# Performance work log

Measured on AMD Instinct MI355X. Metric: run time of the kernel, lower is better.

Reference implementation:

```python
import jax, jax.numpy as jnp
import numpy as np

GAMMA = 1.0
ALPHA = 0.5
EMBED_DIM = 256
N = 8192
M = 8192


def setup_inputs() -> dict:
    key = jax.random.key(0)
    k1, k2, k3, k4 = jax.random.split(key, 4)
    a = jax.random.normal(k1, (N, EMBED_DIM), dtype=jnp.float32)
    b = jax.random.normal(k2, (M, EMBED_DIM), dtype=jnp.float32)
    # torch.nn.Linear default init: U(-1/sqrt(fan_in), 1/sqrt(fan_in))
    lim = 1.0 / np.sqrt(EMBED_DIM)
    Wq = jax.random.uniform(k3, (EMBED_DIM, EMBED_DIM), jnp.float32, -lim, lim)
    Wk = jax.random.uniform(k4, (EMBED_DIM, EMBED_DIM), jnp.float32, -lim, lim)
    return {"a": a, "b": b, "Wq": Wq, "Wk": Wk}


def reference(a, b, Wq, Wk):
    # Vectorized Gram matrix of HybridKernelMethod.forward over all (a_i, b_j) pairs.
    inv_sqrt_d = np.float32(1.0 / np.sqrt(EMBED_DIM))
    ab = a @ b.T                                           # [N, M] cross dot products
    # RBF part: ||a_i - b_j||^2 = ||a_i||^2 + ||b_j||^2 - 2 a_i.b_j
    sq = (jnp.sum(a * a, axis=-1)[:, None]
          + jnp.sum(b * b, axis=-1)[None, :] - 2.0 * ab)
    rbf_sim = jnp.exp(-GAMMA * sq)                         # [N, M]
    # Attention part: per pair, q k^T is a 1x1 matrix, so softmax == 1 exactly.
    q = a @ Wq.T                                           # [N, D]
    k = b @ Wk.T                                           # [M, D]
    s = (q @ k.T) * inv_sqrt_d                             # [N, M] scores
    scores = jax.nn.softmax(s[..., None], axis=-1)[..., 0]  # all-ones, faithful to 1x1 softmax
    attn_sim = scores * ab                                 # sum((scores @ v) * x) == scores * (a.b)
    return (1.0 - ALPHA) * rbf_sim + ALPHA * attn_sim      # [N, M] Gram matrix
```

## Files before the change

kernel.cpp:

```cpp
#include <hip/hip_runtime.h>
#include <stdint.h>

#define DIM 256
#define NR 8192
#define BM 128
#define BN 128
#define BK 64
#define TPB 8
#define GRID 512

typedef __bf16 bf16x8 __attribute__((ext_vector_type(8)));
typedef float  f32x16 __attribute__((ext_vector_type(16)));
typedef float  f32x4  __attribute__((ext_vector_type(4)));

#define MEMFENCE asm volatile("" ::: "memory")
#define WAITV(N) asm volatile("s_waitcnt vmcnt(" #N ")" ::: "memory")

__device__ __forceinline__ unsigned short f2bf_rne(float f) {
    unsigned int u = __float_as_uint(f);
    u += 0x7FFFu + ((u >> 16) & 1u);
    return (unsigned short)(u >> 16);
}

__global__ void prep_kernel(const float* __restrict__ a,
                            const float* __restrict__ b,
                            unsigned short* __restrict__ aB,
                            unsigned short* __restrict__ bB,
                            float* __restrict__ na,
                            float* __restrict__ nb) {
    const int w = threadIdx.x >> 6;
    const int l = threadIdx.x & 63;
    const int blk = blockIdx.x;
    const float* src; unsigned short* dst; float* nrm; int row;
    if (blk < 2048) { src = a; dst = aB; nrm = na; row = blk * 4 + w; }
    else            { src = b; dst = bB; nrm = nb; row = (blk - 2048) * 4 + w; }
    const float4 v = reinterpret_cast<const float4*>(src + (size_t)row * DIM)[l];
    float ss = v.x * v.x + v.y * v.y + v.z * v.z + v.w * v.w;
#pragma unroll
    for (int off = 32; off > 0; off >>= 1) ss += __shfl_down(ss, off);
    if (l == 0) nrm[row] = ss;
    ushort4 o = make_ushort4(f2bf_rne(v.x), f2bf_rne(v.y), f2bf_rne(v.z), f2bf_rne(v.w));
    reinterpret_cast<ushort4*>(dst + (size_t)row * DIM)[l] = o;
}

#define STAGE(row0_, kt_, buf_)                                                   \
    do {                                                                          \
        _Pragma("unroll")                                                         \
        for (int it_ = 0; it_ < 4; ++it_) {                                       \
            __builtin_amdgcn_global_load_lds(                                     \
                (const __attribute__((address_space(1))) void*)(aB +              \
                    (size_t)((row0_) + rowIt[it_]) * DIM + (kt_) * BK + colIt[it_]), \
                (__attribute__((address_space(3))) void*)&sA[buf_][(w * 4 + it_) * 512], \
                16, 0, 0);                                                        \
        }                                                                         \
        _Pragma("unroll")                                                         \
        for (int it_ = 0; it_ < 4; ++it_) {                                       \
            __builtin_amdgcn_global_load_lds(                                     \
                (const __attribute__((address_space(1))) void*)(bB +              \
                    (size_t)(col0 + rowIt[it_]) * DIM + (kt_) * BK + colIt[it_]), \
                (__attribute__((address_space(3))) void*)&sB[buf_][(w * 4 + it_) * 512], \
                16, 0, 0);                                                        \
        }                                                                         \
    } while (0)

#define COMPUTE(buf_)                                                             \
    do {                                                                          \
        _Pragma("unroll")                                                         \
        for (int ks_ = 0; ks_ < 4; ++ks_) {                                       \
            bf16x8 af[2], bfv[2];                                                 \
            _Pragma("unroll")                                                     \
            for (int mi_ = 0; mi_ < 2; ++mi_)                                     \
                af[mi_] = *(const bf16x8*)((const char*)&sA[buf_][0] +            \
                    baseA[mi_] + ((XA[mi_] ^ (ks_ << 1)) << 4));                  \
            _Pragma("unroll")                                                     \
            for (int ni_ = 0; ni_ < 2; ++ni_)                                     \
                bfv[ni_] = *(const bf16x8*)((const char*)&sB[buf_][0] +           \
                    baseB[ni_] + ((XB[ni_] ^ (ks_ << 1)) << 4));                  \
            _Pragma("unroll")                                                     \
            for (int mi_ = 0; mi_ < 2; ++mi_)                                     \
                _Pragma("unroll")                                                 \
                for (int ni_ = 0; ni_ < 2; ++ni_)                                 \
                    acc[mi_][ni_] = __builtin_amdgcn_mfma_f32_32x32x16_bf16(      \
                        af[mi_], bfv[ni_], acc[mi_][ni_], 0, 0, 0);               \
        }                                                                         \
    } while (0)

__global__ __launch_bounds__(256, 2) void gemm_kernel(
        const unsigned short* __restrict__ aB,
        const unsigned short* __restrict__ bB,
        const float* __restrict__ na,
        const float* __restrict__ nb,
        float* __restrict__ out) {
    __shared__ unsigned short sA[2][8192];
    __shared__ unsigned short sB[2][8192];

    const int t = threadIdx.x;
    const int w = t >> 6, l = t & 63;
    const int wr = w >> 1, wc = w & 1;
    const int hi = l >> 5, lr = l & 31;

    const int bx = (int)blockIdx.x & 63;
    const int bb = (int)blockIdx.x >> 6;
    const int col0 = bx * BN;

    int rowIt[4], colIt[4];
#pragma unroll
    for (int it = 0; it < 4; ++it) {
        int G = (w * 4 + it) * 64 + l;
        int rp = G >> 4, pos = G & 15;
        int c2 = pos ^ (rp & 15);
        rowIt[it] = 2 * rp + (c2 >> 3);
        colIt[it] = (c2 & 7) * 8;
    }
    int baseA[2], XA[2], baseB[2], XB[2];
#pragma unroll
    for (int mi = 0; mi < 2; ++mi) {
        int r = wr * 64 + mi * 32 + lr;
        baseA[mi] = (r >> 1) * 256;
        XA[mi] = (((r & 1) * 8) | hi) ^ ((r >> 1) & 15);
        int rb = wc * 64 + mi * 32 + lr;
        baseB[mi] = (rb >> 1) * 256;
        XB[mi] = (((rb & 1) * 8) | hi) ^ ((rb >> 1) & 15);
    }

    float nbv[2];
#pragma unroll
    for (int ni = 0; ni < 2; ++ni) nbv[ni] = nb[col0 + wc * 64 + ni * 32 + lr];

    float outB[2][16];
    f32x4 nav[2][4];

    {
        const int r0 = bb * BM;
        STAGE(r0, 0, 0);
        STAGE(r0, 1, 1);
    }
    MEMFENCE;

    for (int ti = 0; ti < TPB; ++ti) {
        const int row0 = (bb + ti * 8) * BM;
        f32x16 acc[2][2];
#pragma unroll
        for (int mi = 0; mi < 2; ++mi)
#pragma unroll
            for (int ni = 0; ni < 2; ++ni) acc[mi][ni] = (f32x16)0.0f;

        if (ti == 0) { WAITV(0); } else { WAITV(32); }
        __builtin_amdgcn_s_barrier(); MEMFENCE;
        COMPUTE(0);
        MEMFENCE; __builtin_amdgcn_s_barrier(); MEMFENCE;
        STAGE(row0, 2, 0);
        MEMFENCE;
        if (ti > 0) {
            const int prow = row0 - 1024 + wr * 64 + 32 + 4 * hi;
            const int pcol = col0 + wc * 64 + lr;
#pragma unroll
            for (int ni = 0; ni < 2; ++ni)
#pragma unroll
                for (int tt = 0; tt < 16; ++tt) {
                    int q = tt & 3, p = tt >> 2;
                    __builtin_nontemporal_store(outB[ni][tt],
                        &out[(size_t)(prow + 8 * p + q) * 8192 + pcol + ni * 32]);
                }
        }
        MEMFENCE;

        __builtin_amdgcn_s_barrier(); MEMFENCE;
        COMPUTE(1);
        MEMFENCE; __builtin_amdgcn_s_barrier(); MEMFENCE;
        STAGE(row0, 3, 1);
        MEMFENCE;

        if (ti == 0) { WAITV(8); } else { WAITV(40); }
        __builtin_amdgcn_s_barrier(); MEMFENCE;
        COMPUTE(0);
        MEMFENCE; __builtin_amdgcn_s_barrier(); MEMFENCE;
#pragma unroll
        for (int mi = 0; mi < 2; ++mi)
#pragma unroll
            for (int p = 0; p < 4; ++p)
                nav[mi][p] = *(const f32x4*)&na[row0 + wr * 64 + mi * 32 + 8 * p + 4 * hi];
        MEMFENCE;
        if (ti < TPB - 1) STAGE(row0 + 1024, 0, 0);
        MEMFENCE;

        if (ti == TPB - 1) { WAITV(8); } else { WAITV(16); }
        __builtin_amdgcn_s_barrier(); MEMFENCE;
        COMPUTE(1);
        MEMFENCE; __builtin_amdgcn_s_barrier(); MEMFENCE;
        if (ti < TPB - 1) STAGE(row0 + 1024, 1, 1);
        MEMFENCE;

#pragma unroll
        for (int mi = 0; mi < 2; ++mi)
#pragma unroll
            for (int ni = 0; ni < 2; ++ni)
#pragma unroll
                for (int tt = 0; tt < 16; ++tt) {
                    int q = tt & 3, p = tt >> 2;
                    int row = row0 + wr * 64 + mi * 32 + 8 * p + 4 * hi + q;
                    int col = col0 + wc * 64 + ni * 32 + lr;
                    float dot = acc[mi][ni][tt];
                    float sq = nav[mi][p][q] + nbv[ni] - 2.0f * dot;
                    float v = 0.5f * __expf(-sq) + 0.5f * dot;
                    if (mi == 0)
                        __builtin_nontemporal_store(v, &out[(size_t)row * 8192 + col]);
                    else
                        outB[ni][tt] = v;
                }
        MEMFENCE;
    }

    {
        const int prow = (bb + 56) * BM + wr * 64 + 32 + 4 * hi;
        const int pcol = col0 + wc * 64 + lr;
#pragma unroll
        for (int ni = 0; ni < 2; ++ni)
#pragma unroll
            for (int tt = 0; tt < 16; ++tt) {
                int q = tt & 3, p = tt >> 2;
                __builtin_nontemporal_store(outB[ni][tt],
                    &out[(size_t)(prow + 8 * p + q) * 8192 + pcol + ni * 32]);
            }
    }
}

__global__ void naive_kernel(const float* __restrict__ a,
                             const float* __restrict__ b,
                             float* __restrict__ out) {
    const size_t idx = (size_t)blockIdx.x * 256 + threadIdx.x;
    const int i = (int)(idx >> 13);
    const int j = (int)(idx & 8191);
    float dot = 0.f, naa = 0.f, nbb = 0.f;
    for (int k = 0; k < DIM; ++k) {
        const float x = a[(size_t)i * DIM + k];
        const float y = b[(size_t)j * DIM + k];
        dot += x * y; naa += x * x; nbb += y * y;
    }
    const float sq = naa + nbb - 2.0f * dot;
    out[idx] = 0.5f * __expf(-sq) + 0.5f * dot;
}

extern "C" void kernel_launch(void* const* d_in, const int* in_sizes, int n_in,
                              void* d_out, int out_size, void* d_ws, size_t ws_size,
                              hipStream_t stream) {
    const float* a = (const float*)d_in[0];
    const float* b = (const float*)d_in[1];
    float* out = (float*)d_out;

    const size_t bf_bytes = (size_t)NR * DIM * sizeof(unsigned short);
    const size_t nrm_bytes = (size_t)NR * sizeof(float);
    const size_t need = 2 * bf_bytes + 2 * nrm_bytes;

    if (ws_size >= need) {
        unsigned short* aBf = (unsigned short*)d_ws;
        unsigned short* bBf = (unsigned short*)((char*)d_ws + bf_bytes);
        float* na = (float*)((char*)d_ws + 2 * bf_bytes);
        float* nb = (float*)((char*)d_ws + 2 * bf_bytes + nrm_bytes);

        prep_kernel<<<4096, 256, 0, stream>>>(a, b, aBf, bBf, na, nb);
        gemm_kernel<<<GRID, 256, 0, stream>>>(aBf, bBf, na, nb, out);
    } else {
        naive_kernel<<<((size_t)NR * NR) / 256, 256, 0, stream>>>(a, b, out);
    }
}
```

Measured before the change: 77.17 us.

## Defer all output stores into next tile's K-steps and preload row norms to LDS

All four output sub-tiles are now buffered in registers and written out in chunks interleaved after each of the next tile's four compute phases, instead of storing half immediately. Row norms for all tiles of a block are loaded once into LDS at kernel start, replacing per-tile global loads. MFMA sections are wrapped in s_setprio to favour compute waves. The aim is to spread the large output write traffic evenly across the MFMA work. In exchange, register pressure rises (64 buffered floats) and the vmcnt wait counts are retuned by hand, which risks waiting on the wrong loads if miscounted.

```diff
diff --git a/kernel.cpp b/kernel.cpp
--- a/kernel.cpp
+++ b/kernel.cpp
@@ -15,6 +15,7 @@
 
 #define MEMFENCE asm volatile("" ::: "memory")
 #define WAITV(N) asm volatile("s_waitcnt vmcnt(" #N ")" ::: "memory")
+#define BAR __builtin_amdgcn_s_barrier()
 
 __device__ __forceinline__ unsigned short f2bf_rne(float f) {
     unsigned int u = __float_as_uint(f);
@@ -65,6 +66,7 @@
 
 #define COMPUTE(buf_)                                                             \
     do {                                                                          \
+        __builtin_amdgcn_s_setprio(1);                                            \
         _Pragma("unroll")                                                         \
         for (int ks_ = 0; ks_ < 4; ++ks_) {                                       \
             bf16x8 af[2], bfv[2];                                                 \
@@ -83,6 +85,20 @@
                     acc[mi_][ni_] = __builtin_amdgcn_mfma_f32_32x32x16_bf16(      \
                         af[mi_], bfv[ni_], acc[mi_][ni_], 0, 0, 0);               \
         }                                                                         \
+        __builtin_amdgcn_s_setprio(0);                                            \
+    } while (0)
+
+#define STORE_CHUNK(c_, base_)                                                    \
+    do {                                                                          \
+        const int mi_ = (c_) >> 1, ni_ = (c_) & 1;                                \
+        const int prow_ = (base_) + wr * 64 + mi_ * 32 + 4 * hi;                  \
+        const int pcol_ = col0 + wc * 64 + ni_ * 32 + lr;                         \
+        _Pragma("unroll")                                                         \
+        for (int tt_ = 0; tt_ < 16; ++tt_) {                                      \
+            const int q_ = tt_ & 3, p_ = tt_ >> 2;                                \
+            __builtin_nontemporal_store(outB[c_][tt_],                            \
+                &out[(size_t)(prow_ + 8 * p_ + q_) * 8192 + pcol_]);              \
+        }                                                                         \
     } while (0)
 
 __global__ __launch_bounds__(256, 2) void gemm_kernel(
@@ -93,6 +109,7 @@
         float* __restrict__ out) {
     __shared__ unsigned short sA[2][8192];
     __shared__ unsigned short sB[2][8192];
+    __shared__ float sNA[1024];
 
     const int t = threadIdx.x;
     const int w = t >> 6, l = t & 63;
@@ -127,14 +144,16 @@
 #pragma unroll
     for (int ni = 0; ni < 2; ++ni) nbv[ni] = nb[col0 + wc * 64 + ni * 32 + lr];
 
-    float outB[2][16];
-    f32x4 nav[2][4];
-
+    float outB[4][16];
+
+    const f32x4 naIn = *(const f32x4*)&na[(bb + (t >> 5) * 8) * 128 + (t & 31) * 4];
     {
         const int r0 = bb * BM;
         STAGE(r0, 0, 0);
         STAGE(r0, 1, 1);
     }
+    *(f32x4*)&sNA[(t >> 5) * 128 + (t & 31) * 4] = naIn;
+    asm volatile("s_waitcnt lgkmcnt(0)" ::: "memory");
     MEMFENCE;
 
     for (int ti = 0; ti < TPB; ++ti) {
@@ -145,83 +164,63 @@
 #pragma unroll
             for (int ni = 0; ni < 2; ++ni) acc[mi][ni] = (f32x16)0.0f;
 
-        if (ti == 0) { WAITV(0); } else { WAITV(32); }
-        __builtin_amdgcn_s_barrier(); MEMFENCE;
+        if (ti <= 1) { WAITV(8); } else { WAITV(40); }
+        BAR; MEMFENCE;
         COMPUTE(0);
-        MEMFENCE; __builtin_amdgcn_s_barrier(); MEMFENCE;
+        MEMFENCE; BAR; MEMFENCE;
         STAGE(row0, 2, 0);
         MEMFENCE;
-        if (ti > 0) {
-            const int prow = row0 - 1024 + wr * 64 + 32 + 4 * hi;
-            const int pcol = col0 + wc * 64 + lr;
+        if (ti > 0) STORE_CHUNK(0, row0 - 1024);
+        MEMFENCE;
+
+        if (ti == 0) { WAITV(8); } else if (ti == 1) { WAITV(24); } else { WAITV(40); }
+        BAR; MEMFENCE;
+        COMPUTE(1);
+        MEMFENCE; BAR; MEMFENCE;
+        STAGE(row0, 3, 1);
+        MEMFENCE;
+        if (ti > 0) STORE_CHUNK(1, row0 - 1024);
+        MEMFENCE;
+
+        if (ti == 0) { WAITV(8); } else { WAITV(40); }
+        BAR; MEMFENCE;
+        COMPUTE(0);
+        MEMFENCE; BAR; MEMFENCE;
+        if (ti < TPB - 1) STAGE(row0 + 1024, 0, 0);
+        MEMFENCE;
+        if (ti > 0) STORE_CHUNK(2, row0 - 1024);
+        MEMFENCE;
+
+        if (ti == 0) { WAITV(8); } else if (ti == TPB - 1) { WAITV(32); } else { WAITV(40); }
+        BAR; MEMFENCE;
+        COMPUTE(1);
+        MEMFENCE; BAR; MEMFENCE;
+        if (ti < TPB - 1) STAGE(row0 + 1024, 1, 1);
+        MEMFENCE;
+        if (ti > 0) STORE_CHUNK(3, row0 - 1024);
+        MEMFENCE;
+
+#pragma unroll
+        for (int mi = 0; mi < 2; ++mi)
 #pragma unroll
             for (int ni = 0; ni < 2; ++ni)
 #pragma unroll
-                for (int tt = 0; tt < 16; ++tt) {
-                    int q = tt & 3, p = tt >> 2;
-                    __builtin_nontemporal_store(outB[ni][tt],
-                        &out[(size_t)(prow + 8 * p + q) * 8192 + pcol + ni * 32]);
+                for (int p = 0; p < 4; ++p) {
+                    const f32x4 nv = *(const f32x4*)&sNA[ti * 128 + wr * 64 + mi * 32 + 8 * p + 4 * hi];
+#pragma unroll
+                    for (int q = 0; q < 4; ++q) {
+                        const float dot = acc[mi][ni][p * 4 + q];
+                        const float sq = nv[q] + nbv[ni] - 2.0f * dot;
+                        outB[mi * 2 + ni][p * 4 + q] = 0.5f * __expf(-sq) + 0.5f * dot;
+                    }
                 }
-        }
-        MEMFENCE;
-
-        __builtin_amdgcn_s_barrier(); MEMFENCE;
-        COMPUTE(1);
-        MEMFENCE; __builtin_amdgcn_s_barrier(); MEMFENCE;
-        STAGE(row0, 3, 1);
-        MEMFENCE;
-
-        if (ti == 0) { WAITV(8); } else { WAITV(40); }
-        __builtin_amdgcn_s_barrier(); MEMFENCE;
-        COMPUTE(0);
-        MEMFENCE; __builtin_amdgcn_s_barrier(); MEMFENCE;
-#pragma unroll
-        for (int mi = 0; mi < 2; ++mi)
-#pragma unroll
-            for (int p = 0; p < 4; ++p)
-                nav[mi][p] = *(const f32x4*)&na[row0 + wr * 64 + mi * 32 + 8 * p + 4 * hi];
-        MEMFENCE;
-        if (ti < TPB - 1) STAGE(row0 + 1024, 0, 0);
-        MEMFENCE;
-
-        if (ti == TPB - 1) { WAITV(8); } else { WAITV(16); }
-        __builtin_amdgcn_s_barrier(); MEMFENCE;
-        COMPUTE(1);
-        MEMFENCE; __builtin_amdgcn_s_barrier(); MEMFENCE;
-        if (ti < TPB - 1) STAGE(row0 + 1024, 1, 1);
-        MEMFENCE;
-
-#pragma unroll
-        for (int mi = 0; mi < 2; ++mi)
-#pragma unroll
-            for (int ni = 0; ni < 2; ++ni)
-#pragma unroll
-                for (int tt = 0; tt < 16; ++tt) {
-                    int q = tt & 3, p = tt >> 2;
-                    int row = row0 + wr * 64 + mi * 32 + 8 * p + 4 * hi + q;
-                    int col = col0 + wc * 64 + ni * 32 + lr;
-                    float dot = acc[mi][ni][tt];
-                    float sq = nav[mi][p][q] + nbv[ni] - 2.0f * dot;
-                    float v = 0.5f * __expf(-sq) + 0.5f * dot;
-                    if (mi == 0)
-                        __builtin_nontemporal_store(v, &out[(size_t)row * 8192 + col]);
-                    else
-                        outB[ni][tt] = v;
-                }
         MEMFENCE;
     }
 
     {
-        const int prow = (bb + 56) * BM + wr * 64 + 32 + 4 * hi;
-        const int pcol = col0 + wc * 64 + lr;
-#pragma unroll
-        for (int ni = 0; ni < 2; ++ni)
-#pragma unroll
-            for (int tt = 0; tt < 16; ++tt) {
-                int q = tt & 3, p = tt >> 2;
-                __builtin_nontemporal_store(outB[ni][tt],
-                    &out[(size_t)(prow + 8 * p + q) * 8192 + pcol + ni * 32]);
-            }
+        const int base = (bb + 56) * BM;
+#pragma unroll
+        for (int c = 0; c < 4; ++c) STORE_CHUNK(c, base);
     }
 }
 
```

Result: no change. 78.57 us (+1.8%).
